# Kernel optimization log

Measured on AMD Instinct MI355X. Metric: run time of the kernel, lower is better.

## Reference

```python
import jax, jax.numpy as jnp
import numpy as np

B, S, D, H = 2, 2048, 1024, 16
DK = D // H
SCALE = DK ** 0.5


def setup_inputs() -> dict:
    key = jax.random.key(0)
    ks = jax.random.split(key, 5)
    std = 1.0 / np.sqrt(D)
    return {
        "x": jax.random.normal(ks[0], (B, S, D), dtype=jnp.float32),
        "Wq": jax.random.normal(ks[1], (D, D), dtype=jnp.float32) * std,
        "Wk": jax.random.normal(ks[2], (D, D), dtype=jnp.float32) * std,
        "Wv": jax.random.normal(ks[3], (D, D), dtype=jnp.float32) * std,
        "Wo": jax.random.normal(ks[4], (D, D), dtype=jnp.float32) * std,
    }


def _split_heads(t):
    # [B, S, D] -> [B, H, S, DK]
    b, s, d = t.shape
    return t.reshape(b, s, H, DK).transpose(0, 2, 1, 3)


def reference(x, Wq, Wk, Wv, Wo):
    b, s, d = x.shape
    q = _split_heads(x @ Wq)
    k = _split_heads(x @ Wk)
    v = _split_heads(x @ Wv)
    # scores: [B, H, S, S]
    score = jnp.einsum("bhqd,bhkd->bhqk", q, k)
    causal = jnp.tril(jnp.ones((s, s), dtype=bool))[None, None]
    score = jnp.where(causal, score, -jnp.inf)
    attn = jax.nn.softmax(score / SCALE, axis=-1)
    out = jnp.einsum("bhqk,bhkd->bhqd", attn, v)
    out = out.transpose(0, 2, 1, 3).reshape(b, s, d)
    return out @ Wo
```

## Files before the change

### kernel.cpp

```cpp
#include <hip/hip_runtime.h>
#include <hip/hip_bf16.h>

typedef __bf16 bf16;
typedef __bf16 bf16x4 __attribute__((ext_vector_type(4)));
typedef __bf16 bf16x8 __attribute__((ext_vector_type(8)));
typedef float f32x4 __attribute__((ext_vector_type(4)));

#define MFMA16(a, b, c) __builtin_amdgcn_mfma_f32_16x16x32_bf16((a), (b), (c), 0, 0, 0)

__device__ __forceinline__ void async16(const void* g, void* l) {
  typedef const unsigned int __attribute__((address_space(1))) * GP;
  typedef unsigned int __attribute__((address_space(3))) * LP;
  __builtin_amdgcn_global_load_lds((GP)g, (LP)l, 16, 0, 0);
}

__global__ __launch_bounds__(256) void prep(
    const float* __restrict__ w0, const float* __restrict__ w1,
    const float* __restrict__ w2, const float* __restrict__ w3,
    const float* __restrict__ x, bf16* __restrict__ wtOut,
    bf16* __restrict__ xOut) {
  const int t = threadIdx.x;
  if (blockIdx.z == 4) {
    size_t base = ((size_t)(blockIdx.y * 16 + blockIdx.x)) * 16384;
#pragma unroll
    for (int p = 0; p < 16; ++p) {
      size_t i = base + (size_t)(p * 256 + t) * 4;
      f32x4 v = *(const f32x4*)&x[i];
      bf16 o[4];
#pragma unroll
      for (int j = 0; j < 4; ++j) o[j] = (bf16)v[j];
      *(ulong1*)&xOut[i] = *(ulong1*)o;
    }
    return;
  }
  __shared__ __align__(16) float tile[64][68];
  const float* src = (blockIdx.z == 0) ? w0 : (blockIdx.z == 1) ? w1
                   : (blockIdx.z == 2) ? w2 : w3;
  bf16* dst = wtOut + (size_t)blockIdx.z * (1024u * 1024u);
  const int bx = blockIdx.x, by = blockIdx.y;
#pragma unroll
  for (int p = 0; p < 4; ++p) {
    int idx = t + p * 256;
    int r = idx >> 4, c4 = idx & 15;
    *(f32x4*)&tile[r][c4 * 4] =
        *(const f32x4*)&src[(size_t)(by * 64 + r) * 1024 + bx * 64 + c4 * 4];
  }
  __syncthreads();
#pragma unroll
  for (int p = 0; p < 2; ++p) {
    int idx = t + p * 256;
    int rn = idx >> 3, c8 = idx & 7;
    bf16x8 v;
#pragma unroll
    for (int i = 0; i < 8; ++i) v[i] = (bf16)tile[c8 * 8 + i][rn];
    *(bf16x8*)&dst[(size_t)(bx * 64 + rn) * 1024 + by * 64 + c8 * 8] = v;
  }
}

template <typename OutT, int NI>
__global__ __launch_bounds__(256, 4) void gemm_bt(
    const bf16* __restrict__ A, const bf16* __restrict__ Bt,
    OutT* __restrict__ C, int btStrideZ, int cStrideZ, float scaleZ0,
    bf16* __restrict__ vtOut) {
  constexpr int XT = 1024 / (NI * 32);
  const int bid = blockIdx.x;
  const int rr = bid & 7, tt = bid >> 3;
  const int xb = tt % XT, yb = (tt / XT) * 8 + rr;
  const int zi = blockIdx.y;

  const int tid = threadIdx.x;
  const int wave = tid >> 6, lane = tid & 63;
  const int quad = lane >> 4, l16 = lane & 15;
  const int wm = wave >> 1, wn = wave & 1;
  const int m0 = yb * 128, n0 = xb * (NI * 32);
  const bf16* Bz = Bt + (size_t)zi * (size_t)btStrideZ;
  OutT* Cz = C + (size_t)zi * (size_t)cStrideZ;
  const float sc = (zi == 0) ? scaleZ0 : 1.0f;

  __shared__ __align__(16) bf16 lsA[2][128 * 32];
  __shared__ __align__(16) bf16 lsB[2][NI * 32 * 32];

  const int lrow = lane >> 2;
  const int cgX = (lane & 3) ^ ((lrow >> 1) & 3);
  const int fR = (l16 >> 1) & 3;

  f32x4 acc[4][NI];
#pragma unroll
  for (int i = 0; i < 4; ++i)
#pragma unroll
    for (int j = 0; j < NI; ++j) acc[i][j] = (f32x4){0.f, 0.f, 0.f, 0.f};

#pragma unroll
  for (int c = 0; c < 2; ++c) {
    int chunk = wave * 2 + c;
    int row = chunk * 16 + lrow;
    async16(&A[(size_t)(m0 + row) * 1024 + cgX * 8], &lsA[0][chunk * 512]);
  }
#pragma unroll
  for (int c = 0; c < NI / 2; ++c) {
    int chunk = wave * (NI / 2) + c;
    int row = chunk * 16 + lrow;
    async16(&Bz[(size_t)(n0 + row) * 1024 + cgX * 8], &lsB[0][chunk * 512]);
  }
  __syncthreads();

  for (int it = 0; it < 32; ++it) {
    const int cur = it & 1;
    if (it < 31) {
      int k0n = (it + 1) * 32;
#pragma unroll
      for (int c = 0; c < 2; ++c) {
        int chunk = wave * 2 + c;
        int row = chunk * 16 + lrow;
        async16(&A[(size_t)(m0 + row) * 1024 + k0n + cgX * 8],
                &lsA[cur ^ 1][chunk * 512]);
      }
#pragma unroll
      for (int c = 0; c < NI / 2; ++c) {
        int chunk = wave * (NI / 2) + c;
        int row = chunk * 16 + lrow;
        async16(&Bz[(size_t)(n0 + row) * 1024 + k0n + cgX * 8],
                &lsB[cur ^ 1][chunk * 512]);
      }
    }

    bf16x8 af[4], bfr[NI];
#pragma unroll
    for (int i = 0; i < 4; ++i) {
      int ra = wm * 64 + i * 16 + l16;
      af[i] = *(const bf16x8*)&lsA[cur][ra * 32 + ((quad ^ fR) * 8)];
    }
#pragma unroll
    for (int ni = 0; ni < NI; ++ni) {
      int rb = wn * (NI * 16) + ni * 16 + l16;
      bfr[ni] = *(const bf16x8*)&lsB[cur][rb * 32 + ((quad ^ fR) * 8)];
    }
#pragma unroll
    for (int mi = 0; mi < 4; ++mi)
#pragma unroll
      for (int ni = 0; ni < NI; ++ni)
        acc[mi][ni] = MFMA16(af[mi], bfr[ni], acc[mi][ni]);

    __syncthreads();
  }

  if (zi == 2 && vtOut != nullptr) {
#pragma unroll
    for (int mi = 0; mi < 4; ++mi)
#pragma unroll
      for (int ni = 0; ni < NI; ++ni) {
        int col = n0 + wn * (NI * 16) + ni * 16 + l16;
        int h = col >> 6, d = col & 63;
        int row = m0 + wm * 64 + mi * 16 + quad * 4;
        int b = row >> 11, s = row & 2047;
        bf16 o[4];
#pragma unroll
        for (int r = 0; r < 4; ++r) o[r] = (bf16)acc[mi][ni][r];
        *(ulong1*)&vtOut[((size_t)(b * 16 + h) * 64 + d) * 2048 + s] =
            *(ulong1*)o;
      }
  } else {
#pragma unroll
    for (int mi = 0; mi < 4; ++mi)
#pragma unroll
      for (int ni = 0; ni < NI; ++ni) {
        int col = n0 + wn * (NI * 16) + ni * 16 + l16;
#pragma unroll
        for (int r = 0; r < 4; ++r) {
          int row = m0 + wm * 64 + mi * 16 + quad * 4 + r;
          Cz[(size_t)row * 1024 + col] = (OutT)(acc[mi][ni][r] * sc);
        }
      }
  }
}

__global__ __launch_bounds__(512, 4) void attn_fwd(
    const bf16* __restrict__ Q, const bf16* __restrict__ K,
    const bf16* __restrict__ Vt, bf16* __restrict__ O) {
  const int bid = blockIdx.x;
  const int x = bid & 15, hb = bid >> 4;
  const int h = hb & 15, b = hb >> 4;
  const int qt = b ? (15 - x) : x;
  const int tid = threadIdx.x;
  const int wave = tid >> 6, lane = tid & 63;
  const int quad = lane >> 4, l16 = lane & 15;

  __shared__ __align__(16) bf16 SMEM[16384];
  const int kof[2] = {0, 8192};
  const int vof[2] = {4096, 12288};
  bf16* Qs = &SMEM[8192];

  const size_t base = ((size_t)b * 2048) * 1024 + (size_t)h * 64;
  const bf16* Qb = Q + base;
  const bf16* Kb = K + base;
  const bf16* Vtb = Vt + ((size_t)(b * 16 + h)) * 64 * 2048;
  bf16* Ob = O + base;

  const int lrow = lane >> 3;
  const int cgX = (lane & 7) ^ lrow;

#pragma unroll
  for (int c = 0; c < 2; ++c) {
    int chunk = wave * 2 + c;
    int row = chunk * 8 + lrow;
    async16(&Qb[(size_t)(qt * 128 + row) * 1024 + cgX * 8], &Qs[chunk * 512]);
  }
  {
    int row = wave * 8 + lrow;
    async16(&Kb[(size_t)row * 1024 + cgX * 8], &SMEM[kof[0] + wave * 512]);
    async16(&Vtb[(size_t)row * 2048 + cgX * 8], &SMEM[vof[0] + wave * 512]);
  }
  __syncthreads();

  bf16x8 aq[2];
#pragma unroll
  for (int ks = 0; ks < 2; ++ks) {
    int row = wave * 16 + l16;
    aq[ks] = *(const bf16x8*)&Qs[row * 64 + (((ks * 4 + quad) ^ (l16 & 7)) * 8)];
  }
  __syncthreads();

  const float NEG_INF = -__builtin_inff();
  float ls_acc = 0.f;
  f32x4 Oacc[4];
#pragma unroll
  for (int nt = 0; nt < 4; ++nt) Oacc[nt] = (f32x4){0.f, 0.f, 0.f, 0.f};

  const int kt_end = 2 * qt + 1;
  const int ktd = 2 * qt + (wave >> 2);

  for (int kt = 0; kt <= kt_end; ++kt) {
    const int cur = kt & 1;
    if (kt < kt_end) {
      int row = wave * 8 + lrow;
      async16(&Kb[(size_t)((kt + 1) * 64 + row) * 1024 + cgX * 8],
              &SMEM[kof[cur ^ 1] + wave * 512]);
      async16(&Vtb[(size_t)row * 2048 + (kt + 1) * 64 + cgX * 8],
              &SMEM[vof[cur ^ 1] + wave * 512]);
    }

    if (kt <= ktd) {
      f32x4 sv[4];
#pragma unroll
      for (int nt = 0; nt < 4; ++nt) {
        int row = nt * 16 + l16;
        bf16x8 bk0 = *(const bf16x8*)&SMEM[kof[cur] + row * 64 +
                                           ((quad ^ (l16 & 7)) * 8)];
        bf16x8 bk1 = *(const bf16x8*)&SMEM[kof[cur] + row * 64 +
                                           (((4 + quad) ^ (l16 & 7)) * 8)];
        sv[nt] = (f32x4){0.f, 0.f, 0.f, 0.f};
        sv[nt] = MFMA16(bk0, aq[0], sv[nt]);
        sv[nt] = MFMA16(bk1, aq[1], sv[nt]);
      }

      if (kt == ktd) {
        const int q_rel = wave * 16 + l16;
        const int cb = (kt - 2 * qt) * 64;
#pragma unroll
        for (int nt = 0; nt < 4; ++nt) {
          const int kb = cb + nt * 16 + quad * 4;
#pragma unroll
          for (int r = 0; r < 4; ++r)
            if (kb + r > q_rel) sv[nt][r] = NEG_INF;
        }
      }

      bf16x8 apf[2];
#pragma unroll
      for (int a = 0; a < 2; ++a)
#pragma unroll
        for (int g = 0; g < 2; ++g)
#pragma unroll
          for (int r = 0; r < 4; ++r) {
            float p = exp2f(sv[a * 2 + g][r]);
            ls_acc += p;
            apf[a][g * 4 + r] = (bf16)p;
          }

#pragma unroll
      for (int nt = 0; nt < 4; ++nt) {
        const int R = nt * 16 + l16;
        const int sub = (quad & 1) * 4;
#pragma unroll
        for (int a = 0; a < 2; ++a) {
          const int g0 = a * 4 + (quad >> 1);
          const int g1 = g0 + 2;
          bf16x4 lo = *(const bf16x4*)&SMEM[vof[cur] + R * 64 +
                                            ((g0 ^ (l16 & 7)) * 8) + sub];
          bf16x4 hi = *(const bf16x4*)&SMEM[vof[cur] + R * 64 +
                                            ((g1 ^ (l16 & 7)) * 8) + sub];
          bf16x8 bvf;
#pragma unroll
          for (int i = 0; i < 4; ++i) {
            bvf[i] = lo[i];
            bvf[4 + i] = hi[i];
          }
          Oacc[nt] = MFMA16(apf[a], bvf, Oacc[nt]);
        }
      }
    }

    __syncthreads();
  }

  ls_acc += __shfl_xor(ls_acc, 16, 64);
  ls_acc += __shfl_xor(ls_acc, 32, 64);
  float rl[4];
#pragma unroll
  for (int r = 0; r < 4; ++r) rl[r] = 1.f / __shfl(ls_acc, quad * 4 + r, 64);
#pragma unroll
  for (int nt = 0; nt < 4; ++nt)
#pragma unroll
    for (int r = 0; r < 4; ++r) {
      int row = qt * 128 + wave * 16 + quad * 4 + r;
      Ob[(size_t)row * 1024 + nt * 16 + l16] = (bf16)(Oacc[nt][r] * rl[r]);
    }
}

extern "C" void kernel_launch(void* const* d_in, const int* in_sizes, int n_in,
                              void* d_out, int out_size, void* d_ws,
                              size_t ws_size, hipStream_t stream) {
  (void)in_sizes; (void)n_in; (void)out_size; (void)ws_size;
  const float* x  = (const float*)d_in[0];
  const float* Wq = (const float*)d_in[1];
  const float* Wk = (const float*)d_in[2];
  const float* Wv = (const float*)d_in[3];
  const float* Wo = (const float*)d_in[4];
  float* out = (float*)d_out;

  bf16* ws = (bf16*)d_ws;
  const size_t WELEM = 1024u * 1024u;
  const size_t TELEM = 4096u * 1024u;
  bf16* wt  = ws;
  bf16* xbf = ws + 4 * WELEM;
  bf16* q   = xbf + TELEM;
  bf16* k   = q + TELEM;
  bf16* vt  = k + TELEM;
  bf16* ao  = vt + TELEM;

  const float QSCALE = 0.125f * 1.44269504088896340736f;

  prep<<<dim3(16, 16, 5), 256, 0, stream>>>(Wq, Wk, Wv, Wo, x, wt, xbf);
  gemm_bt<bf16, 4><<<dim3(256, 3), 256, 0, stream>>>(
      xbf, wt, q, (int)WELEM, (int)TELEM, QSCALE, vt);
  attn_fwd<<<dim3(512), 512, 0, stream>>>(q, k, vt, ao);
  gemm_bt<float, 2><<<dim3(512, 1), 256, 0, stream>>>(
      ao, wt + 3 * WELEM, out, 0, 0, 1.0f, nullptr);
}
```

Before: 175.3 us.

## Shrink attention query tile to 64 rows with 4 waves and 1024 blocks

The attention kernel now assigns 64 query rows per block using 256 threads (4 waves) instead of 128 rows with 8 waves, doubling the grid to 1024 blocks. Each wave loads two chunks of K/V per step, and the causal masking and per-wave early exit are simplified because the diagonal tile now coincides with the block's query tile. Block indexing is remapped so heads are grouped and the query-tile order alternates direction per group, for load balance. More, smaller blocks should improve occupancy and tail balance, but each K/V tile is now loaded from global memory by twice as many blocks.

```diff
diff --git a/kernel.cpp b/kernel.cpp
--- a/kernel.cpp
+++ b/kernel.cpp
@@ -174,13 +174,14 @@
   }
 }
 
-__global__ __launch_bounds__(512, 4) void attn_fwd(
+__global__ __launch_bounds__(256, 4) void attn_fwd(
     const bf16* __restrict__ Q, const bf16* __restrict__ K,
     const bf16* __restrict__ Vt, bf16* __restrict__ O) {
   const int bid = blockIdx.x;
-  const int x = bid & 15, hb = bid >> 4;
+  const int x = bid & 31, y = (bid >> 5) & 7, p = bid >> 8;
+  const int hb = p * 8 + y;
   const int h = hb & 15, b = hb >> 4;
-  const int qt = b ? (15 - x) : x;
+  const int qt = (p & 1) ? (31 - x) : x;
   const int tid = threadIdx.x;
   const int wave = tid >> 6, lane = tid & 63;
   const int quad = lane >> 4, l16 = lane & 15;
@@ -203,12 +204,11 @@
   for (int c = 0; c < 2; ++c) {
     int chunk = wave * 2 + c;
     int row = chunk * 8 + lrow;
-    async16(&Qb[(size_t)(qt * 128 + row) * 1024 + cgX * 8], &Qs[chunk * 512]);
-  }
-  {
-    int row = wave * 8 + lrow;
-    async16(&Kb[(size_t)row * 1024 + cgX * 8], &SMEM[kof[0] + wave * 512]);
-    async16(&Vtb[(size_t)row * 2048 + cgX * 8], &SMEM[vof[0] + wave * 512]);
+    async16(&Qb[(size_t)(qt * 64 + row) * 1024 + cgX * 8], &Qs[chunk * 512]);
+    async16(&Kb[(size_t)row * 1024 + cgX * 8],
+            &SMEM[kof[0] + chunk * 512]);
+    async16(&Vtb[(size_t)row * 2048 + cgX * 8],
+            &SMEM[vof[0] + chunk * 512]);
   }
   __syncthreads();
 
@@ -226,77 +226,75 @@
 #pragma unroll
   for (int nt = 0; nt < 4; ++nt) Oacc[nt] = (f32x4){0.f, 0.f, 0.f, 0.f};
 
-  const int kt_end = 2 * qt + 1;
-  const int ktd = 2 * qt + (wave >> 2);
-
-  for (int kt = 0; kt <= kt_end; ++kt) {
+  for (int kt = 0; kt <= qt; ++kt) {
     const int cur = kt & 1;
-    if (kt < kt_end) {
-      int row = wave * 8 + lrow;
-      async16(&Kb[(size_t)((kt + 1) * 64 + row) * 1024 + cgX * 8],
-              &SMEM[kof[cur ^ 1] + wave * 512]);
-      async16(&Vtb[(size_t)row * 2048 + (kt + 1) * 64 + cgX * 8],
-              &SMEM[vof[cur ^ 1] + wave * 512]);
-    }
-
-    if (kt <= ktd) {
-      f32x4 sv[4];
+    if (kt < qt) {
+#pragma unroll
+      for (int c = 0; c < 2; ++c) {
+        int chunk = wave * 2 + c;
+        int row = chunk * 8 + lrow;
+        async16(&Kb[(size_t)((kt + 1) * 64 + row) * 1024 + cgX * 8],
+                &SMEM[kof[cur ^ 1] + chunk * 512]);
+        async16(&Vtb[(size_t)row * 2048 + (kt + 1) * 64 + cgX * 8],
+                &SMEM[vof[cur ^ 1] + chunk * 512]);
+      }
+    }
+
+    f32x4 sv[4];
+#pragma unroll
+    for (int nt = 0; nt < 4; ++nt) {
+      int row = nt * 16 + l16;
+      bf16x8 bk0 = *(const bf16x8*)&SMEM[kof[cur] + row * 64 +
+                                         ((quad ^ (l16 & 7)) * 8)];
+      bf16x8 bk1 = *(const bf16x8*)&SMEM[kof[cur] + row * 64 +
+                                         (((4 + quad) ^ (l16 & 7)) * 8)];
+      sv[nt] = (f32x4){0.f, 0.f, 0.f, 0.f};
+      sv[nt] = MFMA16(bk0, aq[0], sv[nt]);
+      sv[nt] = MFMA16(bk1, aq[1], sv[nt]);
+    }
+
+    if (kt == qt) {
+      const int q_rel = wave * 16 + l16;
 #pragma unroll
       for (int nt = 0; nt < 4; ++nt) {
-        int row = nt * 16 + l16;
-        bf16x8 bk0 = *(const bf16x8*)&SMEM[kof[cur] + row * 64 +
-                                           ((quad ^ (l16 & 7)) * 8)];
-        bf16x8 bk1 = *(const bf16x8*)&SMEM[kof[cur] + row * 64 +
-                                           (((4 + quad) ^ (l16 & 7)) * 8)];
-        sv[nt] = (f32x4){0.f, 0.f, 0.f, 0.f};
-        sv[nt] = MFMA16(bk0, aq[0], sv[nt]);
-        sv[nt] = MFMA16(bk1, aq[1], sv[nt]);
-      }
-
-      if (kt == ktd) {
-        const int q_rel = wave * 16 + l16;
-        const int cb = (kt - 2 * qt) * 64;
-#pragma unroll
-        for (int nt = 0; nt < 4; ++nt) {
-          const int kb = cb + nt * 16 + quad * 4;
-#pragma unroll
-          for (int r = 0; r < 4; ++r)
-            if (kb + r > q_rel) sv[nt][r] = NEG_INF;
+        const int kb = nt * 16 + quad * 4;
+#pragma unroll
+        for (int r = 0; r < 4; ++r)
+          if (kb + r > q_rel) sv[nt][r] = NEG_INF;
+      }
+    }
+
+    bf16x8 apf[2];
+#pragma unroll
+    for (int a = 0; a < 2; ++a)
+#pragma unroll
+      for (int g = 0; g < 2; ++g)
+#pragma unroll
+        for (int r = 0; r < 4; ++r) {
+          float pv = exp2f(sv[a * 2 + g][r]);
+          ls_acc += pv;
+          apf[a][g * 4 + r] = (bf16)pv;
         }
-      }
-
-      bf16x8 apf[2];
-#pragma unroll
-      for (int a = 0; a < 2; ++a)
-#pragma unroll
-        for (int g = 0; g < 2; ++g)
-#pragma unroll
-          for (int r = 0; r < 4; ++r) {
-            float p = exp2f(sv[a * 2 + g][r]);
-            ls_acc += p;
-            apf[a][g * 4 + r] = (bf16)p;
-          }
-
-#pragma unroll
-      for (int nt = 0; nt < 4; ++nt) {
-        const int R = nt * 16 + l16;
-        const int sub = (quad & 1) * 4;
-#pragma unroll
-        for (int a = 0; a < 2; ++a) {
-          const int g0 = a * 4 + (quad >> 1);
-          const int g1 = g0 + 2;
-          bf16x4 lo = *(const bf16x4*)&SMEM[vof[cur] + R * 64 +
-                                            ((g0 ^ (l16 & 7)) * 8) + sub];
-          bf16x4 hi = *(const bf16x4*)&SMEM[vof[cur] + R * 64 +
-                                            ((g1 ^ (l16 & 7)) * 8) + sub];
-          bf16x8 bvf;
-#pragma unroll
-          for (int i = 0; i < 4; ++i) {
-            bvf[i] = lo[i];
-            bvf[4 + i] = hi[i];
-          }
-          Oacc[nt] = MFMA16(apf[a], bvf, Oacc[nt]);
+
+#pragma unroll
+    for (int nt = 0; nt < 4; ++nt) {
+      const int R = nt * 16 + l16;
+      const int sub = (quad & 1) * 4;
+#pragma unroll
+      for (int a = 0; a < 2; ++a) {
+        const int g0 = a * 4 + (quad >> 1);
+        const int g1 = g0 + 2;
+        bf16x4 lo = *(const bf16x4*)&SMEM[vof[cur] + R * 64 +
+                                          ((g0 ^ (l16 & 7)) * 8) + sub];
+        bf16x4 hi = *(const bf16x4*)&SMEM[vof[cur] + R * 64 +
+                                          ((g1 ^ (l16 & 7)) * 8) + sub];
+        bf16x8 bvf;
+#pragma unroll
+        for (int i = 0; i < 4; ++i) {
+          bvf[i] = lo[i];
+          bvf[4 + i] = hi[i];
         }
+        Oacc[nt] = MFMA16(apf[a], bvf, Oacc[nt]);
       }
     }
 
@@ -312,7 +310,7 @@
   for (int nt = 0; nt < 4; ++nt)
 #pragma unroll
     for (int r = 0; r < 4; ++r) {
-      int row = qt * 128 + wave * 16 + quad * 4 + r;
+      int row = qt * 64 + wave * 16 + quad * 4 + r;
       Ob[(size_t)row * 1024 + nt * 16 + l16] = (bf16)(Oacc[nt][r] * rl[r]);
     }
 }
@@ -343,7 +341,7 @@
   prep<<<dim3(16, 16, 5), 256, 0, stream>>>(Wq, Wk, Wv, Wo, x, wt, xbf);
   gemm_bt<bf16, 4><<<dim3(256, 3), 256, 0, stream>>>(
       xbf, wt, q, (int)WELEM, (int)TELEM, QSCALE, vt);
-  attn_fwd<<<dim3(512), 512, 0, stream>>>(q, k, vt, ao);
+  attn_fwd<<<dim3(1024), 256, 0, stream>>>(q, k, vt, ao);
   gemm_bt<float, 2><<<dim3(512, 1), 256, 0, stream>>>(
       ao, wt + 3 * WELEM, out, 0, 0, 1.0f, nullptr);
 }
```

Result: no change. 176.5 us (+0.7%).

## Permute V^T sequence layout so PV operand loads become single 16-byte reads

Applied to the files above, without the earlier changes.

The V-projection epilogue now writes V^T with the sequence index permuted inside each 32-key group. This matches the key order the attention kernel's MFMA A-operand uses, so each B-fragment for the PV product is one 16-byte LDS read instead of two 8-byte reads plus a register shuffle. The softmax exponent and row-sum step is also vectorised: a vector accumulator is reduced once at the end, and conversion to bf16 is done per vector. The producer and consumer layouts are now coupled, so any other reader of V^T would see the permuted order.

```diff
diff --git a/kernel.cpp b/kernel.cpp
--- a/kernel.cpp
+++ b/kernel.cpp
@@ -150,13 +150,15 @@
 #pragma unroll
       for (int ni = 0; ni < NI; ++ni) {
         int col = n0 + wn * (NI * 16) + ni * 16 + l16;
-        int h = col >> 6, d = col & 63;
+        int hd = col >> 6, d = col & 63;
         int row = m0 + wm * 64 + mi * 16 + quad * 4;
         int b = row >> 11, s = row & 2047;
+        int s32 = s & 31;
+        int sp = (s & ~31) + ((s32 & 12) << 1) + ((s32 >> 4) << 2);
         bf16 o[4];
 #pragma unroll
         for (int r = 0; r < 4; ++r) o[r] = (bf16)acc[mi][ni][r];
-        *(ulong1*)&vtOut[((size_t)(b * 16 + h) * 64 + d) * 2048 + s] =
+        *(ulong1*)&vtOut[((size_t)(b * 16 + hd) * 64 + d) * 2048 + sp] =
             *(ulong1*)o;
       }
   } else {
@@ -221,7 +223,7 @@
   __syncthreads();
 
   const float NEG_INF = -__builtin_inff();
-  float ls_acc = 0.f;
+  f32x4 lsv = (f32x4){0.f, 0.f, 0.f, 0.f};
   f32x4 Oacc[4];
 #pragma unroll
   for (int nt = 0; nt < 4; ++nt) Oacc[nt] = (f32x4){0.f, 0.f, 0.f, 0.f};
@@ -265,36 +267,32 @@
         }
       }
 
+#pragma unroll
+      for (int nt = 0; nt < 4; ++nt) {
+#pragma unroll
+        for (int r = 0; r < 4; ++r) sv[nt][r] = exp2f(sv[nt][r]);
+        lsv += sv[nt];
+      }
       bf16x8 apf[2];
 #pragma unroll
-      for (int a = 0; a < 2; ++a)
-#pragma unroll
-        for (int g = 0; g < 2; ++g)
-#pragma unroll
-          for (int r = 0; r < 4; ++r) {
-            float p = exp2f(sv[a * 2 + g][r]);
-            ls_acc += p;
-            apf[a][g * 4 + r] = (bf16)p;
-          }
+      for (int a = 0; a < 2; ++a) {
+        bf16x4 c0 = __builtin_convertvector(sv[2 * a], bf16x4);
+        bf16x4 c1 = __builtin_convertvector(sv[2 * a + 1], bf16x4);
+#pragma unroll
+        for (int i = 0; i < 4; ++i) {
+          apf[a][i] = c0[i];
+          apf[a][4 + i] = c1[i];
+        }
+      }
 
 #pragma unroll
       for (int nt = 0; nt < 4; ++nt) {
         const int R = nt * 16 + l16;
-        const int sub = (quad & 1) * 4;
 #pragma unroll
         for (int a = 0; a < 2; ++a) {
-          const int g0 = a * 4 + (quad >> 1);
-          const int g1 = g0 + 2;
-          bf16x4 lo = *(const bf16x4*)&SMEM[vof[cur] + R * 64 +
-                                            ((g0 ^ (l16 & 7)) * 8) + sub];
-          bf16x4 hi = *(const bf16x4*)&SMEM[vof[cur] + R * 64 +
-                                            ((g1 ^ (l16 & 7)) * 8) + sub];
-          bf16x8 bvf;
-#pragma unroll
-          for (int i = 0; i < 4; ++i) {
-            bvf[i] = lo[i];
-            bvf[4 + i] = hi[i];
-          }
+          bf16x8 bvf = *(const bf16x8*)&SMEM[vof[cur] + R * 64 +
+                                             (((a * 4 + quad) ^ (l16 & 7)) *
+                                              8)];
           Oacc[nt] = MFMA16(apf[a], bvf, Oacc[nt]);
         }
       }
@@ -303,6 +301,7 @@
     __syncthreads();
   }
 
+  float ls_acc = lsv[0] + lsv[1] + lsv[2] + lsv[3];
   ls_acc += __shfl_xor(ls_acc, 16, 64);
   ls_acc += __shfl_xor(ls_acc, 32, 64);
   float rl[4];
```

New measurement: 171.1 us. 1.02x faster.
